# Kernel tuning notes

Hardware: AMD Instinct MI355X
Metric: run time of the kernel (lower is better)

Reference implementation:

```python
import jax, jax.numpy as jnp
import numpy as np

B, N, DIM = 16, 1024, 768
H, HD = 12, 64  # num_heads, head_dim


def rotate_half(x):
    x1, x2 = jnp.split(x, 2, axis=-1)
    return jnp.concatenate((-x2, x1), axis=-1)


def setup_inputs() -> dict:
    key = jax.random.key(0)
    k1, k2, k3, k4, k5 = jax.random.split(key, 5)
    x = jax.random.normal(k1, (B, N, DIM), dtype=jnp.float32)
    # precomputed 2D-RoPE angles for the 32x32 patch grid: (N, head_dim)
    sin = jax.random.uniform(k2, (N, HD), dtype=jnp.float32, minval=-1.0, maxval=1.0)
    cos = jax.random.uniform(k3, (N, HD), dtype=jnp.float32, minval=-1.0, maxval=1.0)
    # params: qkv (no bias), proj (with bias)
    W_qkv = jax.random.normal(k4, (DIM, 3 * H * HD), dtype=jnp.float32) / np.sqrt(DIM)
    W_proj = jax.random.normal(k5, (H * HD, DIM), dtype=jnp.float32) / np.sqrt(H * HD)
    b_proj = jnp.zeros((DIM,), dtype=jnp.float32)
    return {"x": x, "sin": sin, "cos": cos, "W_qkv": W_qkv, "W_proj": W_proj, "b_proj": b_proj}


def reference(x, sin, cos, W_qkv, W_proj, b_proj):
    b, n, _ = x.shape
    qkv = (x @ W_qkv).reshape(b, n, 3, H, HD)
    q, k, v = jnp.moveaxis(qkv, 2, 0)          # each (b, n, H, HD)
    q = jnp.swapaxes(q, 1, 2)                  # (b, H, n, HD)
    k = jnp.swapaxes(k, 1, 2)
    v = jnp.swapaxes(v, 1, 2)
    # RoPE (prefix_tokens=0: apply to all tokens); sin/cos broadcast (n,HD)->(1,1,n,HD)
    s = sin[None, None]
    c = cos[None, None]
    q = q * c + rotate_half(q) * s
    k = k * c + rotate_half(k) * s
    # scaled dot-product attention (non-causal, no mask, no dropout)
    scale = 1.0 / jnp.sqrt(jnp.asarray(HD, dtype=q.dtype))
    scores = jnp.einsum('bhqd,bhkd->bhqk', q, k) * scale
    attn = jax.nn.softmax(scores, axis=-1)
    out = jnp.einsum('bhqk,bhkd->bhqd', attn, v)
    out = jnp.swapaxes(out, 1, 2).reshape(b, n, H * HD)
    return out @ W_proj + b_proj
```

## Files before the change

kernel.cpp:

```cpp
#include <hip/hip_runtime.h>


typedef __attribute__((ext_vector_type(8))) _Float16 fp16x8;
typedef __attribute__((ext_vector_type(4))) _Float16 h4;
typedef __attribute__((ext_vector_type(4))) float f32x4;

#define MFMA16(a, b, c) __builtin_amdgcn_mfma_f32_16x16x32_f16(a, b, c, 0, 0, 0)

__device__ __forceinline__ float fexp2(float x) {
    float r;
    asm volatile("v_exp_f32 %0, %1\n\ts_nop 0" : "=v"(r) : "v"(x));
    return r;
}

__device__ __forceinline__ void gload16(const _Float16* g, _Float16* s) {
    __builtin_amdgcn_global_load_lds(
        (const __attribute__((address_space(1))) unsigned int*)g,
        (__attribute__((address_space(3))) unsigned int*)s, 16, 0, 0);
}

__global__ __launch_bounds__(256) void prep_kernel(
    const float* __restrict__ x, const float* __restrict__ Wqkv,
    const float* __restrict__ Wproj, const float* __restrict__ sinp,
    const float* __restrict__ cosp, _Float16* __restrict__ xf,
    _Float16* __restrict__ wqt, _Float16* __restrict__ wpt,
    float4* __restrict__ tab) {
    __shared__ float tile[32][33];
    const int t = threadIdx.x;
    const int b = blockIdx.x;

    if (b < 12288) {
        int i = b * 256 + t;
        float4 v = ((const float4*)x)[i];
        h4 o;
        o[0] = (_Float16)v.x;
        o[1] = (_Float16)v.y;
        o[2] = (_Float16)v.z;
        o[3] = (_Float16)v.w;
        *(h4*)(xf + (size_t)i * 4) = o;
    } else if (b < 14592) {
        const float* W;
        _Float16* outp;
        int rows, cols, bx, by;
        if (b < 14016) {
            int idx = b - 12288;
            W = Wqkv; outp = wqt; rows = 768; cols = 2304;
            bx = idx % 72; by = idx / 72;
        } else {
            int idx = b - 14016;
            W = Wproj; outp = wpt; rows = 768; cols = 768;
            bx = idx % 24; by = idx / 24;
        }
        const int c0 = bx * 32, r0 = by * 32;
#pragma unroll
        for (int i = 0; i < 4; ++i) {
            int idx = t + i * 256;
            int r = idx >> 5, c = idx & 31;
            tile[r][c] = W[(size_t)(r0 + r) * cols + c0 + c];
        }
        __syncthreads();
#pragma unroll
        for (int i = 0; i < 4; ++i) {
            int idx = t + i * 256;
            int rp = idx >> 5, cp = idx & 31;
            outp[(size_t)(c0 + rp) * rows + r0 + cp] = (_Float16)tile[cp][rp];
        }
    } else {
        int idx = (b - 14592) * 256 + t;
        int n = idx >> 5, d = idx & 31;
        float4 v;
        v.x = cosp[n * 64 + d];
        v.y = sinp[n * 64 + d];
        v.z = cosp[n * 64 + d + 32];
        v.w = sinp[n * 64 + d + 32];
        tab[idx] = v;
    }
}

__device__ __forceinline__ void gemm_core8(
    const _Float16* __restrict__ Ag, const _Float16* __restrict__ Bg,
    _Float16* lds, int m0, int n0, f32x4 (&acc)[4][4]) {
    constexpr int BUF = 12288;
    constexpr int OB = 8192;
    const int t = threadIdx.x, l = t & 63, w = t >> 6;
    const int wr = w >> 1, wc = w & 1;
    const int hi = l >> 4, qL = l & 15;

    const int scol = ((t & 3) ^ ((t >> 3) & 3)) << 3;
    const int srow = t >> 2;

    int afo[4], bfo[4];
#pragma unroll
    for (int i = 0; i < 4; ++i) {
        int r = wr * 64 + i * 16 + qL;
        afo[i] = r * 32 + ((hi ^ ((r >> 1) & 3)) << 3);
        int c = wc * 64 + i * 16 + qL;
        bfo[i] = OB + c * 32 + ((hi ^ ((c >> 1) & 3)) << 3);
    }

    auto stageA = [&](int kt, int b) {
        _Float16* base = lds + b * BUF;
        const int k0 = kt * 32;
        gload16(Ag + (size_t)(m0 + srow) * 768 + k0 + scol,
                base + (w * 16) * 32);
        gload16(Ag + (size_t)(m0 + 128 + srow) * 768 + k0 + scol,
                base + (128 + w * 16) * 32);
    };
    auto stageB = [&](int kt, int b) {
        _Float16* base = lds + b * BUF;
        const int k0 = kt * 32;
        gload16(Bg + (size_t)(n0 + srow) * 768 + k0 + scol,
                base + OB + (w * 16) * 32);
    };

    stageA(0, 0);
    stageB(0, 0);
    stageA(1, 1);
    stageB(1, 1);
    asm volatile("s_waitcnt vmcnt(3)" ::: "memory");
    __builtin_amdgcn_s_barrier();

    for (int kt = 0; kt < 24; ++kt) {
        const int bn = (kt + 2) % 3;
        _Float16* bb = lds + (kt % 3) * BUF;

        if (kt < 22) stageA(kt + 2, bn);
        fp16x8 af[4], bf[4];
#pragma unroll
        for (int j = 0; j < 4; ++j) bf[j] = *(const fp16x8*)(bb + bfo[j]);
#pragma unroll
        for (int i = 0; i < 2; ++i) af[i] = *(const fp16x8*)(bb + afo[i]);
        __builtin_amdgcn_s_barrier();
        asm volatile("s_waitcnt lgkmcnt(0)" ::: "memory");
        __builtin_amdgcn_s_setprio(1);
#pragma unroll
        for (int i = 0; i < 2; ++i)
#pragma unroll
            for (int j = 0; j < 4; ++j) acc[i][j] = MFMA16(af[i], bf[j], acc[i][j]);
        __builtin_amdgcn_s_setprio(0);
        __builtin_amdgcn_s_barrier();

        if (kt < 22) stageB(kt + 2, bn);
#pragma unroll
        for (int i = 2; i < 4; ++i) af[i] = *(const fp16x8*)(bb + afo[i]);
        __builtin_amdgcn_s_barrier();
        asm volatile("s_waitcnt lgkmcnt(0)" ::: "memory");
        __builtin_amdgcn_s_setprio(1);
#pragma unroll
        for (int i = 2; i < 4; ++i)
#pragma unroll
            for (int j = 0; j < 4; ++j) acc[i][j] = MFMA16(af[i], bf[j], acc[i][j]);
        __builtin_amdgcn_s_setprio(0);

        if (kt < 22)
            asm volatile("s_waitcnt vmcnt(3)" ::: "memory");
        else
            asm volatile("s_waitcnt vmcnt(0)" ::: "memory");
        __builtin_amdgcn_s_barrier();
    }
}

__global__ __launch_bounds__(512, 4) void qkv_gemm(
    const _Float16* __restrict__ Ag, const _Float16* __restrict__ Bg,
    const float4* __restrict__ tab, _Float16* __restrict__ Qf,
    _Float16* __restrict__ Kf, _Float16* __restrict__ Vt) {
    __shared__ _Float16 lds[3 * 12288];
    const int t = threadIdx.x, l = t & 63, w = t >> 6;
    const int wr = w >> 1, wc = w & 1;
    const int hi = l >> 4, qL = l & 15;

    const int bid = blockIdx.x;
    const int xcd = bid & 7, local = bid >> 3;
    const int m0 = (xcd * 8 + (local & 7)) * 256;
    const int n0 = (local >> 3) * 128;

    f32x4 acc[4][4];
#pragma unroll
    for (int i = 0; i < 4; ++i)
#pragma unroll
        for (int j = 0; j < 4; ++j) acc[i][j] = (f32x4){0.f, 0.f, 0.f, 0.f};

    gemm_core8(Ag, Bg, lds, m0, n0, acc);

    const int sector = n0 / 768;
    const int hbase = (n0 % 768) >> 6;

    if (sector == 2) {
#pragma unroll
        for (int ms = 0; ms < 4; ++ms) {
            int mlb = wr * 64 + ms * 16 + hi * 4;
#pragma unroll
            for (int ns = 0; ns < 4; ++ns) {
                int col = wc * 64 + ns * 16 + qL;
                h4 pk;
#pragma unroll
                for (int reg = 0; reg < 4; ++reg) pk[reg] = (_Float16)acc[ms][ns][reg];
                *(h4*)&lds[col * 264 + mlb] = pk;
            }
        }
        __syncthreads();
        const int b = m0 >> 10, nst = m0 & 1023;
#pragma unroll
        for (int it = 0; it < 8; ++it) {
            int task = it * 512 + t;
            int j = task & 31, col = task >> 5;
            fp16x8 v = *(const fp16x8*)&lds[col * 264 + j * 8];
            int h = hbase + (col >> 6), d = col & 63;
            *(fp16x8*)(Vt + ((size_t)(b * 12 + h) * 64 + d) * 1024 + nst + j * 8) = v;
        }
    } else {
        const float SC = (sector == 0) ? 0.18033688011f : 1.0f;
#pragma unroll
        for (int ms = 0; ms < 4; ++ms) {
#pragma unroll
            for (int reg = 0; reg < 4; ++reg) {
                int ml = wr * 64 + ms * 16 + hi * 4 + reg;
                int n = (m0 + ml) & 1023;
#pragma unroll
                for (int p = 0; p < 2; ++p) {
                    int d = p * 16 + qL;
                    float4 cs = tab[n * 32 + d];
                    float vlo = acc[ms][p][reg], vhi = acc[ms][p + 2][reg];
                    lds[ml * 136 + wc * 64 + d] =
                        (_Float16)((vlo * cs.x - vhi * cs.y) * SC);
                    lds[ml * 136 + wc * 64 + d + 32] =
                        (_Float16)((vhi * cs.z + vlo * cs.w) * SC);
                }
            }
        }
        __syncthreads();
        _Float16* dst = (sector == 0) ? Qf : Kf;
#pragma unroll
        for (int it = 0; it < 8; ++it) {
            int task = it * 512 + t;
            int j = task & 7;
            int r = (task >> 3) & 255;
            int hf = task >> 11;
            fp16x8 v = *(const fp16x8*)&lds[r * 136 + hf * 64 + j * 8];
            int b = (m0 + r) >> 10, n = (m0 + r) & 1023;
            int h = hbase + hf;
            *(fp16x8*)(dst + ((size_t)(b * 12 + h) * 1024 + n) * 64 + j * 8) = v;
        }
    }
}

__global__ __launch_bounds__(512, 4) void proj_gemm(
    const _Float16* __restrict__ Ag, const _Float16* __restrict__ Bg,
    const float* __restrict__ bias, float* __restrict__ out) {
    __shared__ _Float16 lds[3 * 12288];
    const int t = threadIdx.x, l = t & 63, w = t >> 6;
    const int wr = w >> 1, wc = w & 1;
    const int hi = l >> 4, qL = l & 15;

    const int bid = blockIdx.x;
    const int xcd = bid & 7, local = bid >> 3;
    const int m0 = (xcd * 8 + (local & 7)) * 256;
    const int n0 = (local >> 3) * 128;

    f32x4 acc[4][4];
#pragma unroll
    for (int i = 0; i < 4; ++i)
#pragma unroll
        for (int j = 0; j < 4; ++j) acc[i][j] = (f32x4){0.f, 0.f, 0.f, 0.f};

    gemm_core8(Ag, Bg, lds, m0, n0, acc);

#pragma unroll
    for (int ms = 0; ms < 4; ++ms) {
#pragma unroll
        for (int ns = 0; ns < 4; ++ns) {
            int col = n0 + wc * 64 + ns * 16 + qL;
            float bv = bias[col];
#pragma unroll
            for (int reg = 0; reg < 4; ++reg) {
                int m = m0 + wr * 64 + ms * 16 + hi * 4 + reg;
                out[(size_t)m * 768 + col] = acc[ms][ns][reg] + bv;
            }
        }
    }
}

__global__ __launch_bounds__(256, 3) void attn_kernel(
    const _Float16* __restrict__ Qf, const _Float16* __restrict__ Kfg,
    const _Float16* __restrict__ Vtg, _Float16* __restrict__ aof) {
    __shared__ _Float16 khs[2][64][64];
    __shared__ _Float16 vts[2][64][64];
    __shared__ _Float16 pbuf[4][32][72];

    const int t = threadIdx.x, l = t & 63, w = t >> 6;
    const int flat = blockIdx.x;
    const int xcd = flat & 7, idx = flat >> 3;
    const int bh = xcd * 24 + (idx >> 3);
    const int n0 = (idx & 7) * 128;
    const int bq = bh / 12, hh = bh % 12;
    const size_t base = (size_t)bh << 16;
    const int hi = l >> 4, qL = l & 15;

    fp16x8 qf[2][2];
#pragma unroll
    for (int q2 = 0; q2 < 2; ++q2)
#pragma unroll
        for (int kk = 0; kk < 2; ++kk) {
            size_t off = base + (size_t)(n0 + w * 32 + q2 * 16 + qL) * 64 +
                         kk * 32 + (hi << 3);
            qf[q2][kk] = *(const fp16x8*)(Qf + off);
        }

    const int r0 = w * 16;
    const int srow = l >> 3;
    const int scol = ((l & 7) ^ srow) << 3;
    const _Float16* kf_src = Kfg + base + (size_t)(r0 + srow) * 64 + scol;
    const _Float16* vt_src = Vtg + base + (size_t)(r0 + srow) * 1024 + scol;

    int kfo[4][2];
#pragma unroll
    for (int c = 0; c < 4; ++c)
#pragma unroll
        for (int kk = 0; kk < 2; ++kk) {
            int row = c * 16 + qL;
            int col16 = (kk << 2) | hi;
            kfo[c][kk] = row * 64 + ((col16 ^ (row & 7)) << 3);
        }

    f32x4 ot[4][2];
    float l_part[2] = {0.f, 0.f};
#pragma unroll
    for (int q2 = 0; q2 < 2; ++q2)
#pragma unroll
        for (int dt = 0; dt < 4; ++dt) ot[dt][q2] = (f32x4){0.f, 0.f, 0.f, 0.f};

    auto stage = [&](int kt, int b) {
        const _Float16* ks = kf_src + (size_t)kt * 4096;
        gload16(ks, &khs[b][r0][0]);
        gload16(ks + 512, &khs[b][r0 + 8][0]);
        const _Float16* vs = vt_src + kt * 64;
        gload16(vs, &vts[b][r0][0]);
        gload16(vs + 8 * 1024, &vts[b][r0 + 8][0]);
    };

    stage(0, 0);
    __syncthreads();

    for (int kt = 0; kt < 16; ++kt) {
        const int cur = kt & 1;
        if (kt < 15) stage(kt + 1, cur ^ 1);

        const _Float16* kb = &khs[cur][0][0];
        const _Float16* vb = &vts[cur][0][0];

        f32x4 s[4][2];
#pragma unroll
        for (int c = 0; c < 4; ++c) {
            fp16x8 kf0 = *(const fp16x8*)(kb + kfo[c][0]);
            fp16x8 kf1 = *(const fp16x8*)(kb + kfo[c][1]);
#pragma unroll
            for (int q2 = 0; q2 < 2; ++q2) {
                f32x4 a = (f32x4){0.f, 0.f, 0.f, 0.f};
                a = MFMA16(kf0, qf[q2][0], a);
                a = MFMA16(kf1, qf[q2][1], a);
                s[c][q2] = a;
            }
        }

#pragma unroll
        for (int q2 = 0; q2 < 2; ++q2) {
            const int prow = q2 * 16 + qL;
            float lsum = 0.f;
#pragma unroll
            for (int c = 0; c < 4; ++c) {
                float p0 = fexp2(s[c][q2][0] - 4.0f);
                float p1 = fexp2(s[c][q2][1] - 4.0f);
                float p2 = fexp2(s[c][q2][2] - 4.0f);
                float p3 = fexp2(s[c][q2][3] - 4.0f);
                lsum += (p0 + p1) + (p2 + p3);
                h4 pk;
                pk[0] = (_Float16)p0;
                pk[1] = (_Float16)p1;
                pk[2] = (_Float16)p2;
                pk[3] = (_Float16)p3;
                *(h4*)&pbuf[w][prow][c * 16 + (hi << 2)] = pk;
            }
            l_part[q2] += lsum;
        }

        fp16x8 pf[2][2];
#pragma unroll
        for (int q2 = 0; q2 < 2; ++q2)
#pragma unroll
            for (int ss = 0; ss < 2; ++ss)
                pf[q2][ss] = *(const fp16x8*)&pbuf[w][q2 * 16 + qL][ss * 32 + (hi << 3)];

#pragma unroll
        for (int dt = 0; dt < 4; ++dt) {
            fp16x8 v0 = *(const fp16x8*)(vb + kfo[dt][0]);
            fp16x8 v1 = *(const fp16x8*)(vb + kfo[dt][1]);
#pragma unroll
            for (int q2 = 0; q2 < 2; ++q2) {
                ot[dt][q2] = MFMA16(v0, pf[q2][0], ot[dt][q2]);
                ot[dt][q2] = MFMA16(v1, pf[q2][1], ot[dt][q2]);
            }
        }

        __syncthreads();
    }

#pragma unroll
    for (int q2 = 0; q2 < 2; ++q2) {
        float ls = l_part[q2];
        ls += __shfl_xor(ls, 16);
        ls += __shfl_xor(ls, 32);
        float inv = 1.0f / ls;
        int n = n0 + w * 32 + q2 * 16 + qL;
        size_t rowoff = ((size_t)(bq * 1024 + n)) * 768 + hh * 64 + (hi << 2);
#pragma unroll
        for (int dt = 0; dt < 4; ++dt) {
            h4 r;
#pragma unroll
            for (int reg = 0; reg < 4; ++reg) r[reg] = (_Float16)(ot[dt][q2][reg] * inv);
            *(h4*)(aof + rowoff + dt * 16) = r;
        }
    }
}

extern "C" void kernel_launch(void* const* d_in, const int* in_sizes, int n_in,
                              void* d_out, int out_size, void* d_ws, size_t ws_size,
                              hipStream_t stream) {
    const float* x = (const float*)d_in[0];
    const float* sinp = (const float*)d_in[1];
    const float* cosp = (const float*)d_in[2];
    const float* Wqkv = (const float*)d_in[3];
    const float* Wproj = (const float*)d_in[4];
    const float* bproj = (const float*)d_in[5];
    float* out = (float*)d_out;

    char* ws = (char*)d_ws;
    _Float16* xf  = (_Float16*)(ws);
    _Float16* wqt = (_Float16*)(ws + 25165824);
    _Float16* wpt = (_Float16*)(ws + 28704768);
    _Float16* Qf  = (_Float16*)(ws + 29884416);
    _Float16* Kf  = (_Float16*)(ws + 55050240);
    _Float16* Vt  = (_Float16*)(ws + 80216064);
    float4*   tab = (float4*)(ws + 105381888);
    _Float16* aof = xf;

    prep_kernel<<<14720, 256, 0, stream>>>(x, Wqkv, Wproj, sinp, cosp,
                                           xf, wqt, wpt, tab);
    qkv_gemm<<<1152, 512, 0, stream>>>(xf, wqt, tab, Qf, Kf, Vt);
    attn_kernel<<<1536, 256, 0, stream>>>(Qf, Kf, Vt, aof);
    proj_gemm<<<384, 512, 0, stream>>>(aof, wpt, bproj, out);
}
```

Baseline: 184.9 us.

## Widen QKV GEMM tile to 256x256 with templated core and two-round epilogue

```diff
diff --git a/kernel.cpp b/kernel.cpp
--- a/kernel.cpp
+++ b/kernel.cpp
@@ -77,11 +77,13 @@
     }
 }
 
-__device__ __forceinline__ void gemm_core8(
+template <int BN>
+__device__ __forceinline__ void gemm_core(
     const _Float16* __restrict__ Ag, const _Float16* __restrict__ Bg,
-    _Float16* lds, int m0, int n0, f32x4 (&acc)[4][4]) {
-    constexpr int BUF = 12288;
+    _Float16* lds, int m0, int n0, f32x4 (&acc)[4][BN / 32]) {
+    constexpr int NB = BN / 32;
     constexpr int OB = 8192;
+    constexpr int BUF = 8192 + BN * 32;
     const int t = threadIdx.x, l = t & 63, w = t >> 6;
     const int wr = w >> 1, wc = w & 1;
     const int hi = l >> 4, qL = l & 15;
@@ -89,13 +91,16 @@
     const int scol = ((t & 3) ^ ((t >> 3) & 3)) << 3;
     const int srow = t >> 2;
 
-    int afo[4], bfo[4];
+    int afo[4], bfo[NB];
 #pragma unroll
     for (int i = 0; i < 4; ++i) {
         int r = wr * 64 + i * 16 + qL;
         afo[i] = r * 32 + ((hi ^ ((r >> 1) & 3)) << 3);
-        int c = wc * 64 + i * 16 + qL;
-        bfo[i] = OB + c * 32 + ((hi ^ ((c >> 1) & 3)) << 3);
+    }
+#pragma unroll
+    for (int j = 0; j < NB; ++j) {
+        int c = wc * (BN / 2) + j * 16 + qL;
+        bfo[j] = OB + c * 32 + ((hi ^ ((c >> 1) & 3)) << 3);
     }
 
     auto stageA = [&](int kt, int b) {
@@ -111,13 +116,19 @@
         const int k0 = kt * 32;
         gload16(Bg + (size_t)(n0 + srow) * 768 + k0 + scol,
                 base + OB + (w * 16) * 32);
+        if constexpr (BN == 256)
+            gload16(Bg + (size_t)(n0 + 128 + srow) * 768 + k0 + scol,
+                    base + OB + (128 + w * 16) * 32);
     };
 
     stageA(0, 0);
     stageB(0, 0);
     stageA(1, 1);
     stageB(1, 1);
-    asm volatile("s_waitcnt vmcnt(3)" ::: "memory");
+    if constexpr (BN == 128)
+        asm volatile("s_waitcnt vmcnt(3)" ::: "memory");
+    else
+        asm volatile("s_waitcnt vmcnt(4)" ::: "memory");
     __builtin_amdgcn_s_barrier();
 
     for (int kt = 0; kt < 24; ++kt) {
@@ -125,9 +136,9 @@
         _Float16* bb = lds + (kt % 3) * BUF;
 
         if (kt < 22) stageA(kt + 2, bn);
-        fp16x8 af[4], bf[4];
-#pragma unroll
-        for (int j = 0; j < 4; ++j) bf[j] = *(const fp16x8*)(bb + bfo[j]);
+        fp16x8 af[4], bf[NB];
+#pragma unroll
+        for (int j = 0; j < NB; ++j) bf[j] = *(const fp16x8*)(bb + bfo[j]);
 #pragma unroll
         for (int i = 0; i < 2; ++i) af[i] = *(const fp16x8*)(bb + afo[i]);
         __builtin_amdgcn_s_barrier();
@@ -136,7 +147,7 @@
 #pragma unroll
         for (int i = 0; i < 2; ++i)
 #pragma unroll
-            for (int j = 0; j < 4; ++j) acc[i][j] = MFMA16(af[i], bf[j], acc[i][j]);
+            for (int j = 0; j < NB; ++j) acc[i][j] = MFMA16(af[i], bf[j], acc[i][j]);
         __builtin_amdgcn_s_setprio(0);
         __builtin_amdgcn_s_barrier();
 
@@ -149,22 +160,26 @@
 #pragma unroll
         for (int i = 2; i < 4; ++i)
 #pragma unroll
-            for (int j = 0; j < 4; ++j) acc[i][j] = MFMA16(af[i], bf[j], acc[i][j]);
+            for (int j = 0; j < NB; ++j) acc[i][j] = MFMA16(af[i], bf[j], acc[i][j]);
         __builtin_amdgcn_s_setprio(0);
 
-        if (kt < 22)
-            asm volatile("s_waitcnt vmcnt(3)" ::: "memory");
-        else
+        if (kt < 22) {
+            if constexpr (BN == 128)
+                asm volatile("s_waitcnt vmcnt(3)" ::: "memory");
+            else
+                asm volatile("s_waitcnt vmcnt(4)" ::: "memory");
+        } else {
             asm volatile("s_waitcnt vmcnt(0)" ::: "memory");
+        }
         __builtin_amdgcn_s_barrier();
     }
 }
 
-__global__ __launch_bounds__(512, 4) void qkv_gemm(
+__global__ __launch_bounds__(512, 2) void qkv_gemm(
     const _Float16* __restrict__ Ag, const _Float16* __restrict__ Bg,
     const float4* __restrict__ tab, _Float16* __restrict__ Qf,
     _Float16* __restrict__ Kf, _Float16* __restrict__ Vt) {
-    __shared__ _Float16 lds[3 * 12288];
+    __shared__ _Float16 lds[49152];
     const int t = threadIdx.x, l = t & 63, w = t >> 6;
     const int wr = w >> 1, wc = w & 1;
     const int hi = l >> 4, qL = l & 15;
@@ -172,74 +187,94 @@
     const int bid = blockIdx.x;
     const int xcd = bid & 7, local = bid >> 3;
     const int m0 = (xcd * 8 + (local & 7)) * 256;
-    const int n0 = (local >> 3) * 128;
-
-    f32x4 acc[4][4];
+    const int n0 = (local >> 3) * 256;
+
+    f32x4 acc[4][8];
 #pragma unroll
     for (int i = 0; i < 4; ++i)
 #pragma unroll
-        for (int j = 0; j < 4; ++j) acc[i][j] = (f32x4){0.f, 0.f, 0.f, 0.f};
-
-    gemm_core8(Ag, Bg, lds, m0, n0, acc);
+        for (int j = 0; j < 8; ++j) acc[i][j] = (f32x4){0.f, 0.f, 0.f, 0.f};
+
+    gemm_core<256>(Ag, Bg, lds, m0, n0, acc);
 
     const int sector = n0 / 768;
     const int hbase = (n0 % 768) >> 6;
+    const int b = m0 >> 10, nst = m0 & 1023;
 
     if (sector == 2) {
 #pragma unroll
-        for (int ms = 0; ms < 4; ++ms) {
-            int mlb = wr * 64 + ms * 16 + hi * 4;
-#pragma unroll
-            for (int ns = 0; ns < 4; ++ns) {
-                int col = wc * 64 + ns * 16 + qL;
-                h4 pk;
-#pragma unroll
-                for (int reg = 0; reg < 4; ++reg) pk[reg] = (_Float16)acc[ms][ns][reg];
-                *(h4*)&lds[col * 264 + mlb] = pk;
-            }
-        }
-        __syncthreads();
-        const int b = m0 >> 10, nst = m0 & 1023;
-#pragma unroll
-        for (int it = 0; it < 8; ++it) {
-            int task = it * 512 + t;
-            int j = task & 31, col = task >> 5;
-            fp16x8 v = *(const fp16x8*)&lds[col * 264 + j * 8];
-            int h = hbase + (col >> 6), d = col & 63;
-            *(fp16x8*)(Vt + ((size_t)(b * 12 + h) * 64 + d) * 1024 + nst + j * 8) = v;
+        for (int rnd = 0; rnd < 2; ++rnd) {
+            if (wc == rnd) {
+#pragma unroll
+                for (int ms = 0; ms < 4; ++ms) {
+                    int mlb = wr * 64 + ms * 16 + hi * 4;
+#pragma unroll
+                    for (int ns = 0; ns < 8; ++ns) {
+                        int col = ns * 16 + qL;
+                        h4 pk;
+#pragma unroll
+                        for (int reg = 0; reg < 4; ++reg)
+                            pk[reg] = (_Float16)acc[ms][ns][reg];
+                        *(h4*)&lds[col * 264 + mlb] = pk;
+                    }
+                }
+            }
+            __syncthreads();
+#pragma unroll
+            for (int it = 0; it < 8; ++it) {
+                int task = it * 512 + t;
+                int j = task & 31, col = task >> 5;
+                fp16x8 v = *(const fp16x8*)&lds[col * 264 + j * 8];
+                int ac = rnd * 128 + col;
+                int h = hbase + (ac >> 6), d = ac & 63;
+                *(fp16x8*)(Vt + ((size_t)(b * 12 + h) * 64 + d) * 1024 + nst +
+                           j * 8) = v;
+            }
+            __syncthreads();
         }
     } else {
         const float SC = (sector == 0) ? 0.18033688011f : 1.0f;
-#pragma unroll
-        for (int ms = 0; ms < 4; ++ms) {
-#pragma unroll
-            for (int reg = 0; reg < 4; ++reg) {
-                int ml = wr * 64 + ms * 16 + hi * 4 + reg;
-                int n = (m0 + ml) & 1023;
-#pragma unroll
-                for (int p = 0; p < 2; ++p) {
-                    int d = p * 16 + qL;
-                    float4 cs = tab[n * 32 + d];
-                    float vlo = acc[ms][p][reg], vhi = acc[ms][p + 2][reg];
-                    lds[ml * 136 + wc * 64 + d] =
-                        (_Float16)((vlo * cs.x - vhi * cs.y) * SC);
-                    lds[ml * 136 + wc * 64 + d + 32] =
-                        (_Float16)((vhi * cs.z + vlo * cs.w) * SC);
+        _Float16* dst = (sector == 0) ? Qf : Kf;
+#pragma unroll
+        for (int rnd = 0; rnd < 2; ++rnd) {
+            if (wc == rnd) {
+#pragma unroll
+                for (int ms = 0; ms < 4; ++ms) {
+#pragma unroll
+                    for (int reg = 0; reg < 4; ++reg) {
+                        int ml = wr * 64 + ms * 16 + hi * 4 + reg;
+                        int n = (m0 + ml) & 1023;
+#pragma unroll
+                        for (int hh2 = 0; hh2 < 2; ++hh2) {
+#pragma unroll
+                            for (int p = 0; p < 2; ++p) {
+                                int d = p * 16 + qL;
+                                float4 cs = tab[n * 32 + d];
+                                float vlo = acc[ms][hh2 * 4 + p][reg];
+                                float vhi = acc[ms][hh2 * 4 + p + 2][reg];
+                                lds[ml * 136 + hh2 * 64 + d] =
+                                    (_Float16)((vlo * cs.x - vhi * cs.y) * SC);
+                                lds[ml * 136 + hh2 * 64 + d + 32] =
+                                    (_Float16)((vhi * cs.z + vlo * cs.w) * SC);
+                            }
+                        }
+                    }
                 }
             }
-        }
-        __syncthreads();
-        _Float16* dst = (sector == 0) ? Qf : Kf;
-#pragma unroll
-        for (int it = 0; it < 8; ++it) {
-            int task = it * 512 + t;
-            int j = task & 7;
-            int r = (task >> 3) & 255;
-            int hf = task >> 11;
-            fp16x8 v = *(const fp16x8*)&lds[r * 136 + hf * 64 + j * 8];
-            int b = (m0 + r) >> 10, n = (m0 + r) & 1023;
-            int h = hbase + hf;
-            *(fp16x8*)(dst + ((size_t)(b * 12 + h) * 1024 + n) * 64 + j * 8) = v;
+            __syncthreads();
+#pragma unroll
+            for (int it = 0; it < 8; ++it) {
+                int task = it * 512 + t;
+                int j = task & 7;
+                int r = (task >> 3) & 255;
+                int hf = task >> 11;
+                fp16x8 v = *(const fp16x8*)&lds[r * 136 + hf * 64 + j * 8];
+                int n = (m0 + r) & 1023;
+                int h = hbase + rnd * 2 + hf;
+                *(fp16x8*)(dst + ((size_t)(b * 12 + h) * 1024 + n) * 64 +
+                           j * 8) = v;
+            }
+            __syncthreads();
         }
     }
 }
@@ -263,7 +298,7 @@
 #pragma unroll
         for (int j = 0; j < 4; ++j) acc[i][j] = (f32x4){0.f, 0.f, 0.f, 0.f};
 
-    gemm_core8(Ag, Bg, lds, m0, n0, acc);
+    gemm_core<128>(Ag, Bg, lds, m0, n0, acc);
 
 #pragma unroll
     for (int ms = 0; ms < 4; ++ms) {
@@ -445,7 +480,7 @@
 
     prep_kernel<<<14720, 256, 0, stream>>>(x, Wqkv, Wproj, sinp, cosp,
                                            xf, wqt, wpt, tab);
-    qkv_gemm<<<1152, 512, 0, stream>>>(xf, wqt, tab, Qf, Kf, Vt);
+    qkv_gemm<<<576, 512, 0, stream>>>(xf, wqt, tab, Qf, Kf, Vt);
     attn_kernel<<<1536, 256, 0, stream>>>(Qf, Kf, Vt, aof);
     proj_gemm<<<384, 512, 0, stream>>>(aof, wpt, bproj, out);
 }
```

Measured after the change: 192.6 us. 4.2% more time.
